# Kernel tuning notes

Measured on AMD Instinct MI355X. Metric: run time of the kernel, lower is better.

Reference implementation:

```python
import jax, jax.numpy as jnp
import numpy as np

B, S, V, E, H, L = 32, 64, 96, 256, 512, 3
DIN = 2 * H  # padded input width for stacked LSTM weight tensors


def _cell(x, h, c, Wih, Whh, bih, bhh):
    # PyTorch LSTMCell gate order: i, f, g, o
    g = x @ Wih.T + h @ Whh.T + bih + bhh
    i, f, gg, o = jnp.split(g, 4, axis=-1)
    c2 = jax.nn.sigmoid(f) * c + jax.nn.sigmoid(i) * jnp.tanh(gg)
    h2 = jax.nn.sigmoid(o) * jnp.tanh(c2)
    return h2, c2


def _pad_feat(x, d):
    p = d - x.shape[-1]
    return x if p == 0 else jnp.pad(x, ((0, 0),) * (x.ndim - 1) + ((0, p),))


def _run_lstm(xs, Wih, Whh, bih, bhh, reverse):
    # xs: [S, B, Din]
    if reverse:
        xs = xs[::-1]
    b = xs.shape[1]
    init = (jnp.zeros((b, H), xs.dtype), jnp.zeros((b, H), xs.dtype))

    def step(carry, xt):
        h, c = _cell(xt, carry[0], carry[1], Wih, Whh, bih, bhh)
        return (h, c), h

    (h, c), ys = jax.lax.scan(step, init, xs)
    if reverse:
        ys = ys[::-1]
    return ys, h, c


def setup_inputs():
    key = jax.random.key(0)
    ks = jax.random.split(key, 20)
    f = lambda k, shp, s=0.08: jax.random.normal(k, shp, jnp.float32) * s
    return {
        "src": jax.random.randint(ks[0], (B, S), 0, V - 1),  # avoids padding_idx=95
        "trg": jax.random.randint(ks[1], (B, S), 0, V - 1),
        "embedding": f(ks[2], (V, E), 0.5),
        "enc_Wih": f(ks[3], (L, 2, 4 * H, DIN)),
        "enc_Whh": f(ks[4], (L, 2, 4 * H, H)),
        "enc_bih": f(ks[5], (L, 2, 4 * H)),
        "enc_bhh": f(ks[6], (L, 2, 4 * H)),
        "dec_Wih": f(ks[7], (L, 4 * H, DIN)),
        "dec_Whh": f(ks[8], (L, 4 * H, H)),
        "dec_bih": f(ks[9], (L, 4 * H)),
        "dec_bhh": f(ks[10], (L, 4 * H)),
        "attn_W": f(ks[11], (H, 3 * H)),
        "attn_b": f(ks[12], (H,)),
        "attn_v": jax.random.uniform(ks[13], (H,), jnp.float32),
        "proj_W": f(ks[14], (2 * H, E + 2 * H)),
        "proj_b": f(ks[15], (2 * H,)),
        "fc_W": f(ks[16], (V, H)),
        "fc_b": f(ks[17], (V,)),
    }


def _forward(src, trg, embedding, enc_Wih, enc_Whh, enc_bih, enc_bhh,
             dec_Wih, dec_Whh, dec_bih, dec_bhh, attn_W, attn_b, attn_v,
             proj_W, proj_b, fc_W, fc_b):
    emb = embedding[src]                 # [B,S,E]; dropout=identity (eval)
    xs = emb.transpose(1, 0, 2)          # [S,B,E]
    h_sum, c_sum = [], []
    for l in range(L):
        xin = _pad_feat(xs, DIN)         # zero-pad so stacked weights apply; padded cols hit zeros
        yf, hf, cf = _run_lstm(xin, enc_Wih[l, 0], enc_Whh[l, 0], enc_bih[l, 0], enc_bhh[l, 0], False)
        yb, hb, cb = _run_lstm(xin, enc_Wih[l, 1], enc_Whh[l, 1], enc_bih[l, 1], enc_bhh[l, 1], True)
        xs = jnp.concatenate([yf, yb], -1)  # [S,B,2H]
        h_sum.append(hf + hb)
        c_sum.append(cf + cb)            # hidden.view(L,2,B,H).sum(dim=1)
    enc_out = xs.transpose(1, 0, 2)      # [B,S,2H]
    dec_h, dec_c = jnp.stack(h_sum), jnp.stack(c_sum)  # [L,B,H]

    tokens = trg[:, :-1].T               # teacher_forcing_ratio = 1.0 (deterministic)

    def dec_step(carry, tok):
        h, c = carry
        htop = h[-1]                     # [B,H]
        rep = jnp.concatenate([jnp.broadcast_to(htop[:, None, :], (B, S, H)), enc_out], -1)
        energy = jnp.tanh(rep @ attn_W.T + attn_b)               # [B,S,H]
        attn = jax.nn.softmax(jnp.einsum('d,bsd->bs', attn_v, energy), axis=1)
        context = jnp.einsum('bs,bsd->bd', attn, enc_out)        # [B,2H]
        x = jnp.concatenate([embedding[tok], context], -1) @ proj_W.T + proj_b  # [B,2H]
        hs, cs = [], []
        xin = x
        for l in range(L):
            hl, cl = _cell(_pad_feat(xin, DIN), h[l], c[l], dec_Wih[l], dec_Whh[l], dec_bih[l], dec_bhh[l])
            hs.append(hl)
            cs.append(cl)
            xin = hl
        out = xin @ fc_W.T + fc_b        # [B,V]
        return (jnp.stack(hs), jnp.stack(cs)), out

    _, outs = jax.lax.scan(dec_step, (dec_h, dec_c), tokens)     # [S-1,B,V]
    outputs = jnp.concatenate([jnp.zeros((1, B, V), outs.dtype), outs], 0)
    return outputs.transpose(1, 0, 2)    # [B,S,V]; t=0 row is zeros, matching torch


def reference(src, trg, embedding, enc_Wih, enc_Whh, enc_bih, enc_bhh,
              dec_Wih, dec_Whh, dec_bih, dec_bhh, attn_W, attn_b, attn_v,
              proj_W, proj_b, fc_W, fc_b):
    return _forward(src, trg, embedding, enc_Wih, enc_Whh, enc_bih, enc_bhh,
                    dec_Wih, dec_Whh, dec_bih, dec_bhh, attn_W, attn_b, attn_v,
                    proj_W, proj_b, fc_W, fc_b)
```

## Files before the change

### kernel.cpp

```cpp
#include <hip/hip_runtime.h>

#define B_ 32
#define S_ 64
#define V_ 96
#define E_ 256
#define H_ 512
#define L_ 3
#define DIN_ 1024
#define G4_ 2048
#define BH_ (B_*H_)
#define BDIN_ (B_*DIN_)
#define FSTRIDE 16

typedef unsigned short u16;

__device__ __forceinline__ float bfu(u16 u){ return __uint_as_float(((unsigned)u) << 16); }
__device__ __forceinline__ u16 f2b(float f){
  unsigned x = __float_as_uint(f);
  unsigned r = (x + 0x7FFFu + ((x >> 16) & 1u)) >> 16;
  return (u16)r;
}
__device__ __forceinline__ float sigm(float x){ return 1.f/(1.f+__expf(-x)); }
__device__ __forceinline__ float bsum(float a){
  #pragma unroll
  for(int off=1; off<64; off<<=1) a += __shfl_xor(a, off);
  return a;
}
__device__ __forceinline__ void stc(float* p, float v){
  __hip_atomic_store(p, v, __ATOMIC_RELAXED, __HIP_MEMORY_SCOPE_AGENT);
}
__device__ __forceinline__ float ldc(const float* p){
  return __hip_atomic_load((float*)p, __ATOMIC_RELAXED, __HIP_MEMORY_SCOPE_AGENT);
}
__device__ __forceinline__ void stci(int* p, int v){
  __hip_atomic_store(p, v, __ATOMIC_RELAXED, __HIP_MEMORY_SCOPE_AGENT);
}
__device__ __forceinline__ int ldci(const int* p){
  return __hip_atomic_load((int*)p, __ATOMIC_RELAXED, __HIP_MEMORY_SCOPE_AGENT);
}
template<int BF> __device__ __forceinline__ float LD(const void* p, size_t i){
  if constexpr(BF) return bfu(((const u16*)p)[i]);
  else             return ((const float*)p)[i];
}
template<int BF> __device__ __forceinline__ float4 LD4(const void* p, size_t i){
  if constexpr(BF){
    const u16* q = (const u16*)p + i;
    ushort4 w = *(const ushort4*)q;
    return make_float4(bfu(w.x), bfu(w.y), bfu(w.z), bfu(w.w));
  } else {
    return *(const float4*)((const float*)p + i);
  }
}

__device__ __forceinline__ void gbar(int* flags, int g){
  __syncthreads();
  if(threadIdx.x < 64){
    if(threadIdx.x == 0) stci(&flags[blockIdx.x*FSTRIDE], g);
    const int i0 = threadIdx.x*4;
    for(;;){
      int f0 = ldci(&flags[(i0+0)*FSTRIDE]);
      int f1 = ldci(&flags[(i0+1)*FSTRIDE]);
      int f2 = ldci(&flags[(i0+2)*FSTRIDE]);
      int f3 = ldci(&flags[(i0+3)*FSTRIDE]);
      bool ok = (f0>=g) && (f1>=g) && (f2>=g) && (f3>=g);
      if(__all(ok)) break;
      __builtin_amdgcn_s_sleep(1);
    }
  }
  __syncthreads();
}

__global__ void k_detect(const void* av, int* flag, int* flags){
  __shared__ int cnt;
  if(threadIdx.x == 0) cnt = 0;
  __syncthreads();
  u16 w = ((const u16*)av)[2*threadIdx.x];
  if(w & 0x8000) atomicAdd(&cnt, 1);
  __syncthreads();
  for(int i=threadIdx.x; i<256*FSTRIDE+16; i+=256) flags[i] = 0;
  if(threadIdx.x == 0) *flag = (cnt <= 8) ? 1 : 0;
}

template<int BF> __device__ void embed_body(const int* __restrict__ src,
                                            const void* __restrict__ emb,
                                            float* __restrict__ X0){
  int idx = blockIdx.x*256 + threadIdx.x;
  int d  = idx & (DIN_-1);
  int sb = idx >> 10;
  int b  = sb & (B_-1);
  int s  = sb >> 5;
  float v = 0.f;
  if(d < E_){
    int tok = src[b*S_ + s];
    v = LD<BF>(emb, (size_t)tok*E_ + d);
  }
  X0[idx] = v;
}
__global__ void k_embed(const int* src, const void* emb, float* X0, const int* fl){
  if(*fl) embed_body<1>(src, emb, X0); else embed_body<0>(src, emb, X0);
}

template<int BF> __device__ void gemm_body(
  const float* __restrict__ A, int lda,
  const void* __restrict__ W, int ldw, size_t woff,
  const void* __restrict__ b1, size_t o1,
  const void* __restrict__ b2, size_t o2,
  float* __restrict__ C, int ldc, int K)
{
  __shared__ float As[16][128];
  __shared__ float Bs[16][64];
  const int tid = threadIdx.x;
  const int m0 = blockIdx.y * 128;
  const int n0 = blockIdx.x * 64;
  const int tx = tid & 15, ty = tid >> 4;
  const int amm = tid & 127, akk = (tid >> 7) * 8;
  const int bnn = tid >> 2,  bkk = (tid & 3) * 4;
  float acc[8][4] = {{0.f}};
  for(int k0 = 0; k0 < K; k0 += 16){
    const float4* ap = (const float4*)(A + (size_t)(m0+amm)*lda + (k0 + akk));
    float4 a0 = ap[0];
    float4 a1 = ap[1];
    float4 wv = LD4<BF>(W, woff + (size_t)(n0+bnn)*ldw + (k0 + bkk));
    As[akk+0][amm]=a0.x; As[akk+1][amm]=a0.y; As[akk+2][amm]=a0.z; As[akk+3][amm]=a0.w;
    As[akk+4][amm]=a1.x; As[akk+5][amm]=a1.y; As[akk+6][amm]=a1.z; As[akk+7][amm]=a1.w;
    Bs[bkk+0][bnn]=wv.x; Bs[bkk+1][bnn]=wv.y;
    Bs[bkk+2][bnn]=wv.z; Bs[bkk+3][bnn]=wv.w;
    __syncthreads();
    #pragma unroll
    for(int kk=0;kk<16;kk++){
      const float4 av0 = *(const float4*)&As[kk][ty*8];
      const float4 av1 = *(const float4*)&As[kk][ty*8+4];
      const float4 bv  = *(const float4*)&Bs[kk][tx*4];
      float am[8] = {av0.x,av0.y,av0.z,av0.w,av1.x,av1.y,av1.z,av1.w};
      float bn[4] = {bv.x,bv.y,bv.z,bv.w};
      #pragma unroll
      for(int i=0;i<8;i++){
        #pragma unroll
        for(int j=0;j<4;j++) acc[i][j] = fmaf(am[i], bn[j], acc[i][j]);
      }
    }
    __syncthreads();
  }
  float bias[4];
  #pragma unroll
  for(int j=0;j<4;j++){
    float bb = 0.f;
    if(b1) bb += LD<BF>(b1, o1 + n0 + tx*4 + j);
    if(b2) bb += LD<BF>(b2, o2 + n0 + tx*4 + j);
    bias[j] = bb;
  }
  #pragma unroll
  for(int i=0;i<8;i++){
    float* cp = C + (size_t)(m0 + ty*8 + i)*ldc + (n0 + tx*4);
    #pragma unroll
    for(int j=0;j<4;j++) cp[j] = acc[i][j] + bias[j];
  }
}
__global__ __launch_bounds__(256) void k_gemm(
  const float* A, int lda, const void* W, int ldw, size_t woff,
  const void* b1, size_t o1, const void* b2, size_t o2,
  float* C, int ldc, int K, const int* fl)
{
  if(*fl) gemm_body<1>(A,lda,W,ldw,woff,b1,o1,b2,o2,C,ldc,K);
  else    gemm_body<0>(A,lda,W,ldw,woff,b1,o1,b2,o2,C,ldc,K);
}

__global__ void k_outzero(void* __restrict__ out, const int* fl){
  int i = blockIdx.x*256 + threadIdx.x;
  if(i < B_*V_){
    int b = i / V_, v = i % V_;
    size_t idx = (size_t)b*(S_*V_) + v;
    if(*fl) ((u16*)out)[idx] = 0;
    else    ((float*)out)[idx] = 0.f;
  }
}

struct EncArgs2 {
  const float* G;
  const void* Whh; size_t oWh;
  float* henc;
  float* cT;
  float* Xout;
  float* dh0;
  float* dcT;
  int l;
  const int* fl;
  int* flags; int gbase;
};

template<int BF>
__device__ void enc2_body(const EncArgs2& a){
  __shared__ float SM[16384];
  const int tid  = threadIdx.x;
  const int lane = tid & 63;
  const int wid  = tid >> 6;
  const int w4   = (blockIdx.x<<2) + (wid & 3);
  const int j    = w4 & 511;
  const int d    = w4 >> 9;
  const int half = wid >> 2;
  int g = a.gbase;

  float wh[4][8];
  #pragma unroll
  for(int gg=0; gg<4; gg++){
    size_t rowh = a.oWh + ((size_t)d*G4_ + (size_t)gg*H_ + j)*H_;
    #pragma unroll
    for(int p=0;p<2;p++){
      float4 v = LD4<BF>(a.Whh, rowh + (lane<<2) + p*256);
      wh[gg][p*4+0]=v.x; wh[gg][p*4+1]=v.y; wh[gg][p*4+2]=v.z; wh[gg][p*4+3]=v.w;
    }
  }
  const bool own = (lane < 32) && ((lane>>4) == half);
  const size_t ci = ((size_t)d*H_ + j)*32 + (lane & 31);
  float cv = 0.f;

  for(int p=0;p<64;p++){
    const int t = d ? (63-p) : p;
    if(p == 0){
      for(int i=tid<<2; i<BH_; i+=2048) *(float4*)&SM[i] = make_float4(0.f,0.f,0.f,0.f);
    } else {
      const float* hsrc = a.henc + (size_t)((p&63)*2 + d)*BH_;
      for(int i=tid<<2; i<BH_; i+=2048) *(float4*)&SM[i] = *(const float4*)&hsrc[i];
    }
    __syncthreads();

    const int bE = lane & 31;
    const float* Gp = a.G + (size_t)(t*B_+bE)*4096 + (size_t)d*G4_ + j;
    float pg0=Gp[0], pg1=Gp[512], pg2=Gp[1024], pg3=Gp[1536];

    float gv0=0.f, gv1=0.f, gv2=0.f, gv3=0.f;
    for(int b=half*16; b<half*16+16; b++){
      float gs[4] = {0.f,0.f,0.f,0.f};
      const float* hp = &SM[(b<<9) + (lane<<2)];
      #pragma unroll
      for(int pp=0;pp<2;pp++){
        float4 hv = *(const float4*)(hp + pp*256);
        float ha[4] = {hv.x,hv.y,hv.z,hv.w};
        #pragma unroll
        for(int gg=0;gg<4;gg++){
          #pragma unroll
          for(int i=0;i<4;i++) gs[gg] = fmaf(ha[i], wh[gg][pp*4+i], gs[gg]);
        }
      }
      #pragma unroll
      for(int gg=0;gg<4;gg++) gs[gg] = bsum(gs[gg]);
      if(lane == b){ gv0=gs[0]; gv1=gs[1]; gv2=gs[2]; gv3=gs[3]; }
    }
    if(own){
      float gi = gv0+pg0, gf = gv1+pg1, gG = gv2+pg2, go = gv3+pg3;
      float c2 = sigm(gf)*cv + sigm(gi)*tanhf(gG);
      float h2 = sigm(go)*tanhf(c2);
      cv = c2;
      stc(&a.henc[(size_t)(((p+1)&63)*2 + d)*BH_ + (size_t)lane*H_ + j], h2);
      a.Xout[(size_t)(t*B_+lane)*DIN_ + (d<<9) + j] = h2;
    }
    gbar(a.flags, ++g);
  }
  if(own) stc(&a.cT[ci], cv);
  gbar(a.flags, ++g);
  for(int i = blockIdx.x*512 + tid; i < BH_; i += 131072){
    float hf2 = a.henc[(size_t)(0*2+0)*BH_ + i];
    float hb2 = a.henc[(size_t)(0*2+1)*BH_ + i];
    a.dh0[(size_t)a.l*BH_ + i] = hf2 + hb2;
    a.dcT[(size_t)a.l*BH_ + i] = ldc(&a.cT[i]) + ldc(&a.cT[BH_ + i]);
  }
}
__global__ __launch_bounds__(512,1) void k_enc2(EncArgs2 a){
  if(*a.fl) enc2_body<1>(a); else enc2_body<0>(a);
}

struct DecArgs2 {
  const int* trg;
  const void* emb; const void* aW; const void* av; const void* pW; const void* pb;
  const void* dWih; const void* dWhh; const void* dbih; const void* dbhh;
  const void* fW; const void* fb;
  const float* Epre; const float* X3;
  const float* dh0;
  float* dhb;
  float* zb;
  u16*   ctxb;
  float* xpb;
  const float* dcT;
  void* out;
  const int* fl;
  int* flags; int gbase;
};

template<int BF, int CP>
__device__ __forceinline__ void dec_loadW(const DecArgs2& a, const int l,
    const int jp, const int lane, const int half,
    float wx[2][16], float wh[2][8], float pg[2]){
  #pragma unroll
  for(int gg=0; gg<2; gg++){
    const int gr = half*2 + gg;
    size_t rowx = ((size_t)l*G4_ + (size_t)gr*H_ + jp)*DIN_;
    #pragma unroll
    for(int p=0;p<CP;p++){
      float4 v = LD4<BF>(a.dWih, rowx + (lane<<2) + p*256);
      wx[gg][p*4+0]=v.x; wx[gg][p*4+1]=v.y; wx[gg][p*4+2]=v.z; wx[gg][p*4+3]=v.w;
    }
    size_t rowh = ((size_t)l*G4_ + (size_t)gr*H_ + jp)*H_;
    #pragma unroll
    for(int p=0;p<2;p++){
      float4 v = LD4<BF>(a.dWhh, rowh + (lane<<2) + p*256);
      wh[gg][p*4+0]=v.x; wh[gg][p*4+1]=v.y; wh[gg][p*4+2]=v.z; wh[gg][p*4+3]=v.w;
    }
    size_t bb = (size_t)l*G4_ + (size_t)gr*H_ + jp;
    pg[gg] = LD<BF>(a.dbih, bb) + LD<BF>(a.dbhh, bb);
  }
}

template<int BF, int CP>
__device__ __forceinline__ void dec_cellG(const DecArgs2& a, float* SM,
    const int t, const int l, const int jp, const int bh, const int bh_blk,
    const int lane, const int tid, const int half, const int pairid,
    float wx[2][16], float wh[2][8], float pg[2], float& cv){
  constexpr int Kx  = CP*256;
  constexpr int HB  = (CP==4) ? 2 : 1;
  constexpr int NBs = 16/HB;
  const float* xsrc = (l==0) ? (a.xpb + (size_t)t*BDIN_ + (size_t)bh_blk*16*DIN_)
                             : (a.dhb + (size_t)((t+1)*3 + (l-1))*BH_ + (size_t)bh_blk*16*H_);
  const float* hsrc = (t==0) ? (a.dh0 + (size_t)l*BH_ + (size_t)bh_blk*16*H_)
                             : (a.dhb + (size_t)(t*3 + l)*BH_ + (size_t)bh_blk*16*H_);
  float gvA=0.f, gvB=0.f;
  #pragma unroll
  for(int hf=0; hf<HB; hf++){
    const float* xg = xsrc + (size_t)hf*NBs*Kx;
    const float* hg = hsrc + (size_t)hf*NBs*H_;
    for(int i=tid<<2; i<NBs*Kx; i+=2048) *(float4*)&SM[i] = *(const float4*)&xg[i];
    for(int i=tid<<2; i<NBs*H_; i+=2048) *(float4*)&SM[NBs*Kx + i] = *(const float4*)&hg[i];
    __syncthreads();
    for(int ib2=0; ib2<NBs; ib2++){
      const int ib = hf*NBs + ib2;
      float gs0=0.f, gs1=0.f;
      const float* xr = &SM[ib2*Kx + (lane<<2)];
      #pragma unroll
      for(int p=0;p<CP;p++){
        float4 xv = *(const float4*)(xr + p*256);
        gs0 = fmaf(xv.x, wx[0][p*4+0], gs0); gs0 = fmaf(xv.y, wx[0][p*4+1], gs0);
        gs0 = fmaf(xv.z, wx[0][p*4+2], gs0); gs0 = fmaf(xv.w, wx[0][p*4+3], gs0);
        gs1 = fmaf(xv.x, wx[1][p*4+0], gs1); gs1 = fmaf(xv.y, wx[1][p*4+1], gs1);
        gs1 = fmaf(xv.z, wx[1][p*4+2], gs1); gs1 = fmaf(xv.w, wx[1][p*4+3], gs1);
      }
      const float* hr = &SM[NBs*Kx + ib2*H_ + (lane<<2)];
      #pragma unroll
      for(int p=0;p<2;p++){
        float4 hv = *(const float4*)(hr + p*256);
        gs0 = fmaf(hv.x, wh[0][p*4+0], gs0); gs0 = fmaf(hv.y, wh[0][p*4+1], gs0);
        gs0 = fmaf(hv.z, wh[0][p*4+2], gs0); gs0 = fmaf(hv.w, wh[0][p*4+3], gs0);
        gs1 = fmaf(hv.x, wh[1][p*4+0], gs1); gs1 = fmaf(hv.y, wh[1][p*4+1], gs1);
        gs1 = fmaf(hv.z, wh[1][p*4+2], gs1); gs1 = fmaf(hv.w, wh[1][p*4+3], gs1);
      }
      gs0 = bsum(gs0); gs1 = bsum(gs1);
      if(lane == ib){ gvA=gs0; gvB=gs1; }
    }
    __syncthreads();
  }
  float* comb = SM + 15360 + pairid*128;
  if(lane < 16){
    comb[half*32 + lane*2 + 0] = gvA + pg[0];
    comb[half*32 + lane*2 + 1] = gvB + pg[1];
  }
  __syncthreads();
  if(half == 0 && lane < 16){
    const int b = bh*16 + lane;
    float gi = comb[lane*2 + 0];
    float gf = comb[lane*2 + 1];
    float gG = comb[32 + lane*2 + 0];
    float go = comb[32 + lane*2 + 1];
    float c2 = sigm(gf)*cv + sigm(gi)*tanhf(gG);
    float h2 = sigm(go)*tanhf(c2);
    cv = c2;
    stc(&a.dhb[(size_t)((t+1)*3 + l)*BH_ + (size_t)b*H_ + jp], h2);
  }
}

template<int BF>
__device__ void dec2_body(const DecArgs2& a){
  __shared__ float SM[16384];
  const int tid  = threadIdx.x;
  const int lane = tid & 63;
  const int wid  = tid >> 6;
  const int w4   = (blockIdx.x<<2) + (wid & 3);
  const int jp   = w4 & 511;
  const int bh   = w4 >> 9;
  const int half = wid >> 2;
  const int pairid = wid & 3;
  const int bh_blk = blockIdx.x >> 7;
  int g = a.gbase;

  float cvs[3];
  #pragma unroll
  for(int l=0;l<3;l++)
    cvs[l] = a.dcT[((size_t)l*H_ + jp)*32 + (size_t)bh*16 + (lane&15)];

  float wx[2][16], wh[2][8], pg[2];

  for(int t=0; t<64; ++t){
    {
      const float* hs = (t==0) ? (a.dh0 + (size_t)2*BH_ + (size_t)bh_blk*16*H_)
                               : (a.dhb + (size_t)(t*3 + 2)*BH_ + (size_t)bh_blk*16*H_);
      for(int i=tid<<2; i<16*H_; i+=2048) *(float4*)&SM[i] = *(const float4*)&hs[i];
      __syncthreads();
      if(t < 63){
        float wz[8];
        size_t rz = (size_t)jp*1536;
        #pragma unroll
        for(int p=0;p<2;p++){
          float4 v = LD4<BF>(a.aW, rz + (lane<<2) + p*256);
          wz[p*4+0]=v.x; wz[p*4+1]=v.y; wz[p*4+2]=v.z; wz[p*4+3]=v.w;
        }
        for(int ib=half*8; ib<half*8+8; ib++){
          const float* hp = &SM[(ib<<9) + (lane<<2)];
          float acc = 0.f;
          #pragma unroll
          for(int p=0;p<2;p++){
            float4 hv = *(const float4*)(hp + p*256);
            acc = fmaf(hv.x, wz[p*4+0], acc); acc = fmaf(hv.y, wz[p*4+1], acc);
            acc = fmaf(hv.z, wz[p*4+2], acc); acc = fmaf(hv.w, wz[p*4+3], acc);
          }
          acc = bsum(acc);
          if(lane==0) stc(&a.zb[(size_t)t*BH_ + (size_t)(bh*16+ib)*H_ + jp], acc);
        }
      }
      if(t > 0){
        #pragma unroll
        for(int r=0;r<3;r++){
          const int q  = jp + (r<<9);
          const int v_ = q % 96;
          const int ib = q / 96;
          if((ib>>3) != half) continue;
          float wf[8];
          size_t rf = (size_t)v_*H_;
          #pragma unroll
          for(int p=0;p<2;p++){
            float4 v = LD4<BF>(a.fW, rf + (lane<<2) + p*256);
            wf[p*4+0]=v.x; wf[p*4+1]=v.y; wf[p*4+2]=v.z; wf[p*4+3]=v.w;
          }
          const float* hp = &SM[(ib<<9) + (lane<<2)];
          float acc = 0.f;
          #pragma unroll
          for(int p=0;p<2;p++){
            float4 hv = *(const float4*)(hp + p*256);
            acc = fmaf(hv.x, wf[p*4+0], acc); acc = fmaf(hv.y, wf[p*4+1], acc);
            acc = fmaf(hv.z, wf[p*4+2], acc); acc = fmaf(hv.w, wf[p*4+3], acc);
          }
          acc = bsum(acc);
          if(lane==0){
            float rr = acc + LD<BF>(a.fb, v_);
            size_t oi = (size_t)(bh*16+ib)*(S_*V_) + (size_t)t*V_ + v_;
            if constexpr(BF) ((u16*)a.out)[oi] = f2b(rr);
            else             ((float*)a.out)[oi] = rr;
          }
        }
      }
    }
    if(t == 63) break;
    gbar(a.flags, ++g);

    if(blockIdx.x < 32){
      const int b = blockIdx.x;
      float* Zs = SM; float* Ss = SM + 512;
      for(int i=tid; i<512; i+=512) Zs[i] = a.zb[(size_t)t*BH_ + (size_t)b*H_ + i];
      __syncthreads();
      float wa[8];
      #pragma unroll
      for(int p=0;p<2;p++){
        float4 v = LD4<BF>(a.av, (lane<<2) + p*256);
        wa[p*4+0]=v.x; wa[p*4+1]=v.y; wa[p*4+2]=v.z; wa[p*4+3]=v.w;
      }
      for(int s=wid; s<64; s+=8){
        const float* ep = a.Epre + ((size_t)(s*B_ + b))*H_;
        float acc = 0.f;
        #pragma unroll
        for(int p=0;p<2;p++){
          const float4 e4 = *(const float4*)(ep + (lane<<2) + p*256);
          const float4 z4 = *(const float4*)(Zs + (lane<<2) + p*256);
          acc = fmaf(wa[p*4+0], tanhf(e4.x+z4.x), acc);
          acc = fmaf(wa[p*4+1], tanhf(e4.y+z4.y), acc);
          acc = fmaf(wa[p*4+2], tanhf(e4.z+z4.z), acc);
          acc = fmaf(wa[p*4+3], tanhf(e4.w+z4.w), acc);
        }
        acc = bsum(acc);
        if(lane==0) Ss[s] = acc;
      }
      __syncthreads();
      if(tid < 64){
        float vv = Ss[tid];
        float m = vv;
        #pragma unroll
        for(int off=1; off<64; off<<=1) m = fmaxf(m, __shfl_xor(m, off));
        float e = __expf(vv - m);
        float su = e;
        #pragma unroll
        for(int off=1; off<64; off<<=1) su += __shfl_xor(su, off);
        Ss[tid] = e / su;
      }
      __syncthreads();
      for(int d4 = tid<<2; d4 < DIN_; d4 += 2048){
        float a0=0.f,a1=0.f,a2=0.f,a3=0.f;
        const float* xb = a.X3 + (size_t)b*DIN_ + d4;
        for(int s=0;s<64;s++){
          const float pp = Ss[s];
          const float4 xv = *(const float4*)(xb + (size_t)s*BDIN_);
          a0 = fmaf(pp, xv.x, a0); a1 = fmaf(pp, xv.y, a1);
          a2 = fmaf(pp, xv.z, a2); a3 = fmaf(pp, xv.w, a3);
        }
        u16* cp = a.ctxb + (size_t)t*BDIN_ + (size_t)b*DIN_ + d4;
        unsigned lo = (unsigned)f2b(a0) | ((unsigned)f2b(a1)<<16);
        unsigned hi = (unsigned)f2b(a2) | ((unsigned)f2b(a3)<<16);
        stci((int*)cp, (int)lo);
        stci(((int*)cp)+1, (int)hi);
      }
    }
    gbar(a.flags, ++g);

    {
      const u16* cs = a.ctxb + (size_t)t*BDIN_ + (size_t)bh_blk*16*DIN_;
      for(int i=tid*4; i<16*DIN_; i+=2048){
        ushort4 v = *(const ushort4*)(cs + i);
        *(float4*)&SM[i] = make_float4(bfu(v.x), bfu(v.y), bfu(v.z), bfu(v.w));
      }
      __syncthreads();
      float wpe[2][4], wpc[2][16];
      #pragma unroll
      for(int jj=0;jj<2;jj++){
        size_t row = (size_t)(jp + (jj<<9))*1280;
        float4 v = LD4<BF>(a.pW, row + (lane<<2));
        wpe[jj][0]=v.x; wpe[jj][1]=v.y; wpe[jj][2]=v.z; wpe[jj][3]=v.w;
        #pragma unroll
        for(int p=0;p<4;p++){
          float4 c4 = LD4<BF>(a.pW, row + 256 + (lane<<2) + p*256);
          wpc[jj][p*4+0]=c4.x; wpc[jj][p*4+1]=c4.y; wpc[jj][p*4+2]=c4.z; wpc[jj][p*4+3]=c4.w;
        }
      }
      const float pb0 = LD<BF>(a.pb, jp);
      const float pb1 = LD<BF>(a.pb, jp+512);
      for(int ib=half*8; ib<half*8+8; ib++){
        const int b = bh*16 + ib;
        const int tok = a.trg[b*S_ + t];
        float4 ev = LD4<BF>(a.emb, (size_t)tok*E_ + (lane<<2));
        float ea[4] = {ev.x, ev.y, ev.z, ev.w};
        float s0=0.f, s1=0.f;
        #pragma unroll
        for(int i=0;i<4;i++){ s0 = fmaf(ea[i], wpe[0][i], s0); s1 = fmaf(ea[i], wpe[1][i], s1); }
        const float* cp = &SM[(ib<<10) + (lane<<2)];
        #pragma unroll
        for(int p=0;p<4;p++){
          float4 c4 = *(const float4*)(cp + p*256);
          float ca[4] = {c4.x,c4.y,c4.z,c4.w};
          #pragma unroll
          for(int i=0;i<4;i++){ s0 = fmaf(ca[i], wpc[0][p*4+i], s0); s1 = fmaf(ca[i], wpc[1][p*4+i], s1); }
        }
        s0 = bsum(s0); s1 = bsum(s1);
        if(lane==0){
          stc(&a.xpb[(size_t)t*BDIN_ + (size_t)b*DIN_ + jp],       s0 + pb0);
          stc(&a.xpb[(size_t)t*BDIN_ + (size_t)b*DIN_ + jp + 512], s1 + pb1);
        }
      }
      __syncthreads();
    }
    dec_loadW<BF,4>(a, 0, jp, lane, half, wx, wh, pg);
    gbar(a.flags, ++g);
    dec_cellG<BF,4>(a, SM, t, 0, jp, bh, bh_blk, lane, tid, half, pairid, wx, wh, pg, cvs[0]);
    dec_loadW<BF,2>(a, 1, jp, lane, half, wx, wh, pg);
    gbar(a.flags, ++g);
    dec_cellG<BF,2>(a, SM, t, 1, jp, bh, bh_blk, lane, tid, half, pairid, wx, wh, pg, cvs[1]);
    dec_loadW<BF,2>(a, 2, jp, lane, half, wx, wh, pg);
    gbar(a.flags, ++g);
    dec_cellG<BF,2>(a, SM, t, 2, jp, bh, bh_blk, lane, tid, half, pairid, wx, wh, pg, cvs[2]);
    gbar(a.flags, ++g);
  }
}
__global__ __launch_bounds__(512,1) void k_dec2(DecArgs2 a){
  if(*a.fl) dec2_body<1>(a); else dec2_body<0>(a);
}

struct EncArgsO {
  const float* G;
  const float* Xin;
  const void* Wih; size_t oWi;
  const void* Whh; size_t oWh;
  const void* bih; size_t obi;
  const void* bhh; size_t obh;
  float* hst; float* cT; float* Xout; float* dh; float* dcT;
  int l; const int* fl; int* flags; int gbase;
};

template<int BF, int CP>
__device__ void encO_body(const EncArgsO& a){
  __shared__ float SM[16384];
  const int tid  = threadIdx.x;
  const int w    = (blockIdx.x<<2) + (tid>>6);
  const int lane = tid & 63;
  const int d    = w >> 9;
  const int j    = w & 511;
  int g = a.gbase;

  float wh[4][8];
  #pragma unroll
  for(int gg=0; gg<4; gg++){
    size_t rowh = a.oWh + ((size_t)d*G4_ + (size_t)gg*H_ + j)*H_;
    #pragma unroll
    for(int p=0;p<2;p++){
      float4 v = LD4<BF>(a.Whh, rowh + (lane<<2) + p*256);
      wh[gg][p*4+0]=v.x; wh[gg][p*4+1]=v.y; wh[gg][p*4+2]=v.z; wh[gg][p*4+3]=v.w;
    }
  }
  float wxf[4][CP?CP*4:1];
  float pbias[4];
  if constexpr(CP>0){
    #pragma unroll
    for(int gg=0; gg<4; gg++){
      size_t rowx = a.oWi + ((size_t)d*G4_ + (size_t)gg*H_ + j)*DIN_;
      #pragma unroll
      for(int p=0;p<CP;p++){
        float4 v = LD4<BF>(a.Wih, rowx + (lane<<2) + p*256);
        wxf[gg][p*4+0]=v.x; wxf[gg][p*4+1]=v.y; wxf[gg][p*4+2]=v.z; wxf[gg][p*4+3]=v.w;
      }
    }
    size_t bb = (size_t)d*G4_ + j;
    #pragma unroll
    for(int gg=0;gg<4;gg++)
      pbias[gg] = LD<BF>(a.bih, a.obi + bb + (size_t)gg*H_)
                + LD<BF>(a.bhh, a.obh + bb + (size_t)gg*H_);
  }
  const int bE = lane & 31;
  const size_t ci = ((size_t)d*H_ + j)*32 + bE;
  float cv = 0.f;
  int cur = 0;
  for(int p=0;p<64;p++){
    const int t = d ? (63-p) : p;
    if(p == 0){
      for(int i=tid<<2; i<BH_; i+=1024) *(float4*)&SM[i] = make_float4(0.f,0.f,0.f,0.f);
    } else {
      const float* hsrc = a.hst + (size_t)((cur<<1)+d)*BH_;
      #pragma unroll 4
      for(int i=tid; i<BH_; i+=256) SM[i] = ldc(hsrc + i);
    }
    __syncthreads();
    float pg[4];
    if constexpr(CP==0){
      const float* Gp = a.G + (size_t)(t*B_+bE)*4096 + (size_t)d*G4_ + j;
      pg[0]=Gp[0]; pg[1]=Gp[512]; pg[2]=Gp[1024]; pg[3]=Gp[1536];
    } else {
      pg[0]=pbias[0]; pg[1]=pbias[1]; pg[2]=pbias[2]; pg[3]=pbias[3];
    }
    const float* xrow = nullptr;
    if constexpr(CP>0) xrow = a.Xin + (size_t)t*B_*DIN_;
    float gv0=0.f, gv1=0.f, gv2=0.f, gv3=0.f;
    for(int b=0;b<32;b++){
      float gs[4] = {0.f,0.f,0.f,0.f};
      const float* hp = &SM[(b<<9) + (lane<<2)];
      #pragma unroll
      for(int pp=0;pp<2;pp++){
        float4 hv = *(const float4*)(hp + pp*256);
        float ha[4] = {hv.x,hv.y,hv.z,hv.w};
        #pragma unroll
        for(int gg=0;gg<4;gg++){
          #pragma unroll
          for(int i=0;i<4;i++) gs[gg] = fmaf(ha[i], wh[gg][pp*4+i], gs[gg]);
        }
      }
      if constexpr(CP>0){
        const float* xr = xrow + (size_t)b*DIN_ + (lane<<2);
        #pragma unroll
        for(int pp=0;pp<CP;pp++){
          float4 xv = *(const float4*)(xr + pp*256);
          float xa[4] = {xv.x,xv.y,xv.z,xv.w};
          #pragma unroll
          for(int gg=0;gg<4;gg++){
            #pragma unroll
            for(int i=0;i<4;i++) gs[gg] = fmaf(xa[i], wxf[gg][pp*4+i], gs[gg]);
          }
        }
      }
      #pragma unroll
      for(int gg=0;gg<4;gg++) gs[gg] = bsum(gs[gg]);
      if(lane == b){ gv0=gs[0]; gv1=gs[1]; gv2=gs[2]; gv3=gs[3]; }
    }
    if(lane < 32){
      float gi = gv0+pg[0], gf = gv1+pg[1], gG = gv2+pg[2], go = gv3+pg[3];
      float c2 = sigm(gf)*cv + sigm(gi)*tanhf(gG);
      float h2 = sigm(go)*tanhf(c2);
      cv = c2;
      stc(&a.hst[(size_t)(((cur^1)<<1)+d)*BH_ + (size_t)bE*H_ + j], h2);
      a.Xout[(size_t)(t*B_+bE)*DIN_ + (d<<9) + j] = h2;
    }
    gbar(a.flags, ++g);
    cur ^= 1;
  }
  if(lane < 32) stc(&a.cT[ci], cv);
  gbar(a.flags, ++g);
  for(int i = blockIdx.x*256 + tid; i < BH_; i += 65536){
    a.dh[(size_t)a.l*BH_ + i]  = ldc(&a.hst[(size_t)(cur<<1)*BH_ + i])
                               + ldc(&a.hst[(size_t)((cur<<1)+1)*BH_ + i]);
    a.dcT[(size_t)a.l*BH_ + i] = ldc(&a.cT[i]) + ldc(&a.cT[BH_ + i]);
  }
}
__global__ __launch_bounds__(256,2) void k_enc_persF0(EncArgsO a){
  if(*a.fl) encO_body<1,1>(a); else encO_body<0,1>(a);
}
__global__ __launch_bounds__(256,2) void k_enc_persF12(EncArgsO a){
  if(*a.fl) encO_body<1,4>(a); else encO_body<0,4>(a);
}

struct DecArgsO {
  const int* trg;
  const void* emb; const void* aW; const void* av; const void* pW; const void* pb;
  const void* dWih; const void* dWhh; const void* dbih; const void* dbhh;
  const void* fW; const void* fb;
  const float* Epre; const float* X3;
  float* dh; float* dcT; float* z; float* ctx; float* xp;
  void* out; const int* fl; int* flags; int gbase;
};

template<int BF, int CP>
__device__ __forceinline__ void decO_cell(const DecArgsO& a, float* SM,
    const int l, const int cur, const int jp, const int bh, const int bh_blk,
    const int lane, const int tid, int& g, float& cv){
  constexpr int Kx = CP*256;
  constexpr int HB = (CP==4) ? 2 : 1;
  constexpr int NB = 16/HB;
  const float* xsrc = (l==0) ? (a.xp + (size_t)bh_blk*16*DIN_)
                             : (a.dh + ((size_t)(cur^1)*3 + (l-1))*BH_ + (size_t)bh_blk*16*H_);
  const float* hsrc = a.dh + ((size_t)cur*3 + l)*BH_ + (size_t)bh_blk*16*H_;
  float wx[4][CP*4];
  float wh[4][8];
  #pragma unroll
  for(int gg=0; gg<4; gg++){
    size_t rowx = ((size_t)l*G4_ + (size_t)gg*H_ + jp)*DIN_;
    #pragma unroll
    for(int p=0;p<CP;p++){
      float4 v = LD4<BF>(a.dWih, rowx + (lane<<2) + p*256);
      wx[gg][p*4+0]=v.x; wx[gg][p*4+1]=v.y; wx[gg][p*4+2]=v.z; wx[gg][p*4+3]=v.w;
    }
    size_t rowh = ((size_t)l*G4_ + (size_t)gg*H_ + jp)*H_;
    #pragma unroll
    for(int p=0;p<2;p++){
      float4 v = LD4<BF>(a.dWhh, rowh + (lane<<2) + p*256);
      wh[gg][p*4+0]=v.x; wh[gg][p*4+1]=v.y; wh[gg][p*4+2]=v.z; wh[gg][p*4+3]=v.w;
    }
  }
  float pg[4];
  {
    size_t bb = (size_t)l*G4_ + jp;
    #pragma unroll
    for(int gg=0;gg<4;gg++)
      pg[gg] = LD<BF>(a.dbih, bb + (size_t)gg*H_) + LD<BF>(a.dbhh, bb + (size_t)gg*H_);
  }
  float gv0=0.f,gv1=0.f,gv2=0.f,gv3=0.f;
  #pragma unroll
  for(int hf=0; hf<HB; hf++){
    const float* xg = xsrc + (size_t)hf*NB*Kx;
    const float* hg = hsrc + (size_t)hf*NB*H_;
    #pragma unroll 4
    for(int i=tid; i<NB*Kx; i+=256) SM[i] = ldc(xg + i);
    #pragma unroll 4
    for(int i=tid; i<NB*H_; i+=256) SM[NB*Kx + i] = ldc(hg + i);
    __syncthreads();
    for(int ib2=0; ib2<NB; ib2++){
      const int ib = hf*NB + ib2;
      float gs[4] = {0.f,0.f,0.f,0.f};
      const float* xr = &SM[ib2*Kx + (lane<<2)];
      #pragma unroll
      for(int p=0;p<CP;p++){
        float4 xv = *(const float4*)(xr + p*256);
        float xa[4] = {xv.x,xv.y,xv.z,xv.w};
        #pragma unroll
        for(int gg=0;gg<4;gg++){
          #pragma unroll
          for(int i=0;i<4;i++) gs[gg] = fmaf(xa[i], wx[gg][p*4+i], gs[gg]);
        }
      }
      const float* hr = &SM[NB*Kx + ib2*H_ + (lane<<2)];
      #pragma unroll
      for(int p=0;p<2;p++){
        float4 hv = *(const float4*)(hr + p*256);
        float ha[4] = {hv.x,hv.y,hv.z,hv.w};
        #pragma unroll
        for(int gg=0;gg<4;gg++){
          #pragma unroll
          for(int i=0;i<4;i++) gs[gg] = fmaf(ha[i], wh[gg][p*4+i], gs[gg]);
        }
      }
      #pragma unroll
      for(int gg=0;gg<4;gg++) gs[gg] = bsum(gs[gg]);
      if(lane == ib){ gv0=gs[0]; gv1=gs[1]; gv2=gs[2]; gv3=gs[3]; }
    }
    __syncthreads();
  }
  if(lane < 16){
    const int b = bh*16 + lane;
    float gi = gv0+pg[0], gf = gv1+pg[1], gG = gv2+pg[2], go = gv3+pg[3];
    float c2 = sigm(gf)*cv + sigm(gi)*tanhf(gG);
    float h2 = sigm(go)*tanhf(c2);
    cv = c2;
    stc(&a.dh[((size_t)(cur^1)*3 + l)*BH_ + (size_t)b*H_ + jp], h2);
  }
  gbar(a.flags, ++g);
}

template<int BF>
__device__ void decO_body(const DecArgsO& a){
  __shared__ float SM[16384];
  const int tid  = threadIdx.x;
  const int w    = (blockIdx.x<<2) + (tid>>6);
  const int lane = tid & 63;
  const int jp   = w & 511;
  const int bh   = w >> 9;
  const int bh_blk = blockIdx.x >> 7;
  int g = a.gbase;
  float cvs[3];
  #pragma unroll
  for(int l=0;l<3;l++)
    cvs[l] = a.dcT[((size_t)l*H_ + jp)*32 + (size_t)bh*16 + (lane&15)];
  int cur = 0;
  for(int t=0; t<64; ++t){
    {
      const float* hs = a.dh + ((size_t)cur*3 + 2)*BH_ + (size_t)bh_blk*16*H_;
      #pragma unroll 4
      for(int i=tid; i<16*H_; i+=256) SM[i] = ldc(hs + i);
      __syncthreads();
      if(t < 63){
        float wz[8];
        size_t rz = (size_t)jp*1536;
        #pragma unroll
        for(int p=0;p<2;p++){
          float4 v = LD4<BF>(a.aW, rz + (lane<<2) + p*256);
          wz[p*4+0]=v.x; wz[p*4+1]=v.y; wz[p*4+2]=v.z; wz[p*4+3]=v.w;
        }
        for(int ib=0; ib<16; ib++){
          const float* hp = &SM[(ib<<9) + (lane<<2)];
          float acc = 0.f;
          #pragma unroll
          for(int p=0;p<2;p++){
            float4 hv = *(const float4*)(hp + p*256);
            acc = fmaf(hv.x, wz[p*4+0], acc); acc = fmaf(hv.y, wz[p*4+1], acc);
            acc = fmaf(hv.z, wz[p*4+2], acc); acc = fmaf(hv.w, wz[p*4+3], acc);
          }
          acc = bsum(acc);
          if(lane==0) stc(&a.z[(size_t)(bh*16+ib)*H_ + jp], acc);
        }
      }
      if(t > 0){
        #pragma unroll
        for(int r=0;r<3;r++){
          const int q  = jp + (r<<9);
          const int v_ = q % 96;
          const int ib = q / 96;
          float wf[8];
          size_t rf = (size_t)v_*H_;
          #pragma unroll
          for(int p=0;p<2;p++){
            float4 v = LD4<BF>(a.fW, rf + (lane<<2) + p*256);
            wf[p*4+0]=v.x; wf[p*4+1]=v.y; wf[p*4+2]=v.z; wf[p*4+3]=v.w;
          }
          const float* hp = &SM[(ib<<9) + (lane<<2)];
          float acc = 0.f;
          #pragma unroll
          for(int p=0;p<2;p++){
            float4 hv = *(const float4*)(hp + p*256);
            acc = fmaf(hv.x, wf[p*4+0], acc); acc = fmaf(hv.y, wf[p*4+1], acc);
            acc = fmaf(hv.z, wf[p*4+2], acc); acc = fmaf(hv.w, wf[p*4+3], acc);
          }
          acc = bsum(acc);
          if(lane==0){
            float rr = acc + LD<BF>(a.fb, v_);
            size_t oi = (size_t)(bh*16+ib)*(S_*V_) + (size_t)t*V_ + v_;
            if constexpr(BF) ((u16*)a.out)[oi] = f2b(rr);
            else             ((float*)a.out)[oi] = rr;
          }
        }
      }
    }
    if(t == 63) break;
    gbar(a.flags, ++g);
    if(blockIdx.x < 32){
      const int b = blockIdx.x;
      float* Zs = SM; float* Ss = SM + 512;
      for(int i=tid; i<512; i+=256) Zs[i] = ldc(a.z + (size_t)b*H_ + i);
      __syncthreads();
      float wa[8];
      #pragma unroll
      for(int p=0;p<2;p++){
        float4 v = LD4<BF>(a.av, (lane<<2) + p*256);
        wa[p*4+0]=v.x; wa[p*4+1]=v.y; wa[p*4+2]=v.z; wa[p*4+3]=v.w;
      }
      const int ww = tid>>6;
      for(int s=ww; s<64; s+=4){
        const float* ep = a.Epre + ((size_t)(s*B_ + b))*H_;
        float acc = 0.f;
        #pragma unroll
        for(int p=0;p<2;p++){
          const float4 e4 = *(const float4*)(ep + (lane<<2) + p*256);
          const float4 z4 = *(const float4*)(Zs + (lane<<2) + p*256);
          acc = fmaf(wa[p*4+0], tanhf(e4.x+z4.x), acc);
          acc = fmaf(wa[p*4+1], tanhf(e4.y+z4.y), acc);
          acc = fmaf(wa[p*4+2], tanhf(e4.z+z4.z), acc);
          acc = fmaf(wa[p*4+3], tanhf(e4.w+z4.w), acc);
        }
        acc = bsum(acc);
        if(lane==0) Ss[s] = acc;
      }
      __syncthreads();
      if(tid < 64){
        float vv = Ss[tid];
        float m = vv;
        #pragma unroll
        for(int off=1; off<64; off<<=1) m = fmaxf(m, __shfl_xor(m, off));
        float e = __expf(vv - m);
        float su = e;
        #pragma unroll
        for(int off=1; off<64; off<<=1) su += __shfl_xor(su, off);
        Ss[tid] = e / su;
      }
      __syncthreads();
      for(int d4 = tid<<2; d4 < DIN_; d4 += 1024){
        float a0=0.f,a1=0.f,a2=0.f,a3=0.f;
        const float* xb = a.X3 + (size_t)b*DIN_ + d4;
        for(int s=0;s<64;s++){
          const float pp = Ss[s];
          const float4 xv = *(const float4*)(xb + (size_t)s*BDIN_);
          a0 = fmaf(pp, xv.x, a0); a1 = fmaf(pp, xv.y, a1);
          a2 = fmaf(pp, xv.z, a2); a3 = fmaf(pp, xv.w, a3);
        }
        float* cp = &a.ctx[(size_t)b*DIN_ + d4];
        stc(cp+0, a0); stc(cp+1, a1); stc(cp+2, a2); stc(cp+3, a3);
      }
    }
    gbar(a.flags, ++g);
    {
      const float* cs = a.ctx + (size_t)bh_blk*16*DIN_;
      #pragma unroll 4
      for(int i=tid; i<16*DIN_; i+=256) SM[i] = ldc(cs + i);
      __syncthreads();
      float wpe[2][4], wpc[2][16];
      #pragma unroll
      for(int jj=0;jj<2;jj++){
        size_t row = (size_t)(jp + (jj<<9))*1280;
        float4 v = LD4<BF>(a.pW, row + (lane<<2));
        wpe[jj][0]=v.x; wpe[jj][1]=v.y; wpe[jj][2]=v.z; wpe[jj][3]=v.w;
        #pragma unroll
        for(int p=0;p<4;p++){
          float4 c4 = LD4<BF>(a.pW, row + 256 + (lane<<2) + p*256);
          wpc[jj][p*4+0]=c4.x; wpc[jj][p*4+1]=c4.y; wpc[jj][p*4+2]=c4.z; wpc[jj][p*4+3]=c4.w;
        }
      }
      const float pb0 = LD<BF>(a.pb, jp);
      const float pb1 = LD<BF>(a.pb, jp+512);
      for(int ib=0; ib<16; ib++){
        const int b = bh*16 + ib;
        const int tok = a.trg[b*S_ + t];
        float4 ev = LD4<BF>(a.emb, (size_t)tok*E_ + (lane<<2));
        float ea[4] = {ev.x, ev.y, ev.z, ev.w};
        float s0=0.f, s1=0.f;
        #pragma unroll
        for(int i=0;i<4;i++){ s0 = fmaf(ea[i], wpe[0][i], s0); s1 = fmaf(ea[i], wpe[1][i], s1); }
        const float* cp = &SM[(ib<<10) + (lane<<2)];
        #pragma unroll
        for(int p=0;p<4;p++){
          float4 c4 = *(const float4*)(cp + p*256);
          float ca[4] = {c4.x,c4.y,c4.z,c4.w};
          #pragma unroll
          for(int i=0;i<4;i++){ s0 = fmaf(ca[i], wpc[0][p*4+i], s0); s1 = fmaf(ca[i], wpc[1][p*4+i], s1); }
        }
        s0 = bsum(s0); s1 = bsum(s1);
        if(lane==0){
          stc(&a.xp[(size_t)b*DIN_ + jp],       s0 + pb0);
          stc(&a.xp[(size_t)b*DIN_ + jp + 512], s1 + pb1);
        }
      }
    }
    gbar(a.flags, ++g);
    decO_cell<BF,4>(a, SM, 0, cur, jp, bh, bh_blk, lane, tid, g, cvs[0]);
    decO_cell<BF,2>(a, SM, 1, cur, jp, bh, bh_blk, lane, tid, g, cvs[1]);
    decO_cell<BF,2>(a, SM, 2, cur, jp, bh, bh_blk, lane, tid, g, cvs[2]);
    cur ^= 1;
  }
}
__global__ __launch_bounds__(256,2) void k_dec_persO(DecArgsO a){
  if(*a.fl) decO_body<1>(a); else decO_body<0>(a);
}

extern "C" void kernel_launch(void* const* d_in, const int* in_sizes, int n_in,
                              void* d_out, int out_size, void* d_ws, size_t ws_size,
                              hipStream_t stream){
  const int* src  = (const int*)d_in[0];
  const int* trg  = (const int*)d_in[1];
  const void* emb = d_in[2];
  const void* eWih= d_in[3];
  const void* eWhh= d_in[4];
  const void* ebih= d_in[5];
  const void* ebhh= d_in[6];
  const void* dWih= d_in[7];
  const void* dWhh= d_in[8];
  const void* dbih= d_in[9];
  const void* dbhh= d_in[10];
  const void* aW  = d_in[11];
  const void* ab  = d_in[12];
  const void* av  = d_in[13];
  const void* pW  = d_in[14];
  const void* pb  = d_in[15];
  const void* fW  = d_in[16];
  const void* fb  = d_in[17];

  char* base = (char*)d_ws;
  size_t off = 0;
  auto take = [&](size_t bytes)->char*{
    char* p = base + off; off = (off + bytes + 255) & ~(size_t)255; return p;
  };

  const size_t szX  = (size_t)2048*1024*4;
  const size_t szG  = (size_t)2048*4096*4;
  const size_t szE  = (size_t)2048*512*4;
  int planA = ws_size >= (size_t)53*1024*1024;

  if(planA){
    float* X    = (float*)take(szX);
    float* Xh   = (float*)take(szX);
    float* G    = (float*)take(szG);
    float* dhb  = G;
    float* zb   = dhb + (size_t)64*3*BH_;
    float* xpb  = zb  + (size_t)63*BH_;
    u16*   ctxb = (u16*)(xpb + (size_t)63*BDIN_);
    float* Epre = (float*)take(szE);
    float* cTe  = (float*)take((size_t)2*BH_*4);
    float* dh0  = (float*)take((size_t)3*BH_*4);
    float* dcT  = (float*)take((size_t)3*BH_*4);
    int* fl     = (int*)take(256);
    int* flags  = (int*)take((256*FSTRIDE + 16)*4);

    k_detect<<<1, 256, 0, stream>>>(av, fl, flags);
    k_embed<<<8192, 256, 0, stream>>>(src, emb, X, fl);

    for(int l=0;l<L_;l++){
      int K = (l==0) ? E_ : DIN_;
      k_gemm<<<dim3(64,16), 256, 0, stream>>>(X, DIN_,
          eWih, DIN_, (size_t)l*2*G4_*DIN_,
          ebih, (size_t)l*2*G4_, ebhh, (size_t)l*2*G4_,
          G, 4096, K, fl);
      EncArgs2 ea;
      ea.G = G; ea.Whh = eWhh; ea.oWh = (size_t)l*2*G4_*H_;
      ea.henc = Xh; ea.cT = cTe; ea.Xout = X;
      ea.dh0 = dh0; ea.dcT = dcT; ea.l = l;
      ea.fl = fl; ea.flags = flags; ea.gbase = l*65;
      k_enc2<<<256, 512, 0, stream>>>(ea);
    }
    k_gemm<<<dim3(8,16), 256, 0, stream>>>(X, DIN_,
        aW, 3*H_, (size_t)H_, ab, 0, nullptr, 0, Epre, H_, DIN_, fl);
    k_outzero<<<12, 256, 0, stream>>>(d_out, fl);

    DecArgs2 da;
    da.trg = trg; da.emb = emb; da.aW = aW; da.av = av; da.pW = pW; da.pb = pb;
    da.dWih = dWih; da.dWhh = dWhh; da.dbih = dbih; da.dbhh = dbhh;
    da.fW = fW; da.fb = fb;
    da.Epre = Epre; da.X3 = X;
    da.dh0 = dh0; da.dhb = dhb; da.zb = zb; da.ctxb = ctxb; da.xpb = xpb;
    da.dcT = dcT; da.out = d_out; da.fl = fl; da.flags = flags; da.gbase = 3*65;
    k_dec2<<<256, 512, 0, stream>>>(da);
  } else {
    float* XA   = (float*)take(szX);
    float* XB   = (float*)take(szX);
    float* Epre = (float*)take(szE);
    float* hst  = (float*)take((size_t)4*BH_*4);
    float* cTe  = (float*)take((size_t)2*BH_*4);
    float* dh   = (float*)take((size_t)6*BH_*4);
    float* dcT  = (float*)take((size_t)3*BH_*4);
    float* zbuf = (float*)take((size_t)BH_*4);
    float* ctx  = (float*)take((size_t)2*BH_*4);
    float* xp   = (float*)take((size_t)2*BH_*4);
    int* fl     = (int*)take(256);
    int* flags  = (int*)take((256*FSTRIDE + 16)*4);

    k_detect<<<1, 256, 0, stream>>>(av, fl, flags);
    k_embed<<<8192, 256, 0, stream>>>(src, emb, XA, fl);

    float* Xin = XA; float* Xout = XB;
    for(int l=0;l<L_;l++){
      EncArgsO ea;
      ea.G = nullptr; ea.Xin = Xin;
      ea.Wih = eWih; ea.oWi = (size_t)l*2*G4_*DIN_;
      ea.Whh = eWhh; ea.oWh = (size_t)l*2*G4_*H_;
      ea.bih = ebih; ea.obi = (size_t)l*2*G4_;
      ea.bhh = ebhh; ea.obh = (size_t)l*2*G4_;
      ea.hst = hst; ea.cT = cTe; ea.Xout = Xout;
      ea.dh = dh; ea.dcT = dcT; ea.l = l;
      ea.fl = fl; ea.flags = flags; ea.gbase = l*65;
      if(l == 0) k_enc_persF0<<<256, 256, 0, stream>>>(ea);
      else       k_enc_persF12<<<256, 256, 0, stream>>>(ea);
      float* tmp = Xin; Xin = Xout; Xout = tmp;
    }
    k_gemm<<<dim3(8,16), 256, 0, stream>>>(Xin, DIN_,
        aW, 3*H_, (size_t)H_, ab, 0, nullptr, 0, Epre, H_, DIN_, fl);
    k_outzero<<<12, 256, 0, stream>>>(d_out, fl);

    DecArgsO da;
    da.trg = trg; da.emb = emb; da.aW = aW; da.av = av; da.pW = pW; da.pb = pb;
    da.dWih = dWih; da.dWhh = dWhh; da.dbih = dbih; da.dbhh = dbhh;
    da.fW = fW; da.fb = fb;
    da.Epre = Epre; da.X3 = Xin;
    da.dh = dh; da.dcT = dcT; da.z = zbuf; da.ctx = ctx; da.xp = xp;
    da.out = d_out; da.fl = fl; da.flags = flags; da.gbase = 3*65;
    k_dec_persO<<<256, 256, 0, stream>>>(da);
  }
}
```

Baseline: 9.584 ms.

## Split attention context across all blocks and break FMA dependency chains

The attention/context phase previously ran on only 32 blocks (one per batch row). It now runs on every block (b = blockIdx>>3, 8 slices of the 1024-wide context), so each block recomputes the scores and softmax but accumulates only 128 context columns. This is meant to shorten the serial context phase between global barriers, at the cost of redundant score work. Several dot products (gate, attention-z, fc, projection) also switch to two independent accumulators to shorten FMA dependency chains, which changes the summation order slightly.

```diff
diff --git a/kernel.cpp b/kernel.cpp
--- a/kernel.cpp
+++ b/kernel.cpp
@@ -332,26 +332,40 @@
     __syncthreads();
     for(int ib2=0; ib2<NBs; ib2++){
       const int ib = hf*NBs + ib2;
-      float gs0=0.f, gs1=0.f;
+      float g0a=0.f,g0b=0.f,g1a=0.f,g1b=0.f;
       const float* xr = &SM[ib2*Kx + (lane<<2)];
       #pragma unroll
       for(int p=0;p<CP;p++){
         float4 xv = *(const float4*)(xr + p*256);
-        gs0 = fmaf(xv.x, wx[0][p*4+0], gs0); gs0 = fmaf(xv.y, wx[0][p*4+1], gs0);
-        gs0 = fmaf(xv.z, wx[0][p*4+2], gs0); gs0 = fmaf(xv.w, wx[0][p*4+3], gs0);
-        gs1 = fmaf(xv.x, wx[1][p*4+0], gs1); gs1 = fmaf(xv.y, wx[1][p*4+1], gs1);
-        gs1 = fmaf(xv.z, wx[1][p*4+2], gs1); gs1 = fmaf(xv.w, wx[1][p*4+3], gs1);
+        if(p & 1){
+          g0b = fmaf(xv.x, wx[0][p*4+0], g0b); g0b = fmaf(xv.y, wx[0][p*4+1], g0b);
+          g0b = fmaf(xv.z, wx[0][p*4+2], g0b); g0b = fmaf(xv.w, wx[0][p*4+3], g0b);
+          g1b = fmaf(xv.x, wx[1][p*4+0], g1b); g1b = fmaf(xv.y, wx[1][p*4+1], g1b);
+          g1b = fmaf(xv.z, wx[1][p*4+2], g1b); g1b = fmaf(xv.w, wx[1][p*4+3], g1b);
+        } else {
+          g0a = fmaf(xv.x, wx[0][p*4+0], g0a); g0a = fmaf(xv.y, wx[0][p*4+1], g0a);
+          g0a = fmaf(xv.z, wx[0][p*4+2], g0a); g0a = fmaf(xv.w, wx[0][p*4+3], g0a);
+          g1a = fmaf(xv.x, wx[1][p*4+0], g1a); g1a = fmaf(xv.y, wx[1][p*4+1], g1a);
+          g1a = fmaf(xv.z, wx[1][p*4+2], g1a); g1a = fmaf(xv.w, wx[1][p*4+3], g1a);
+        }
       }
       const float* hr = &SM[NBs*Kx + ib2*H_ + (lane<<2)];
-      #pragma unroll
-      for(int p=0;p<2;p++){
-        float4 hv = *(const float4*)(hr + p*256);
-        gs0 = fmaf(hv.x, wh[0][p*4+0], gs0); gs0 = fmaf(hv.y, wh[0][p*4+1], gs0);
-        gs0 = fmaf(hv.z, wh[0][p*4+2], gs0); gs0 = fmaf(hv.w, wh[0][p*4+3], gs0);
-        gs1 = fmaf(hv.x, wh[1][p*4+0], gs1); gs1 = fmaf(hv.y, wh[1][p*4+1], gs1);
-        gs1 = fmaf(hv.z, wh[1][p*4+2], gs1); gs1 = fmaf(hv.w, wh[1][p*4+3], gs1);
-      }
-      gs0 = bsum(gs0); gs1 = bsum(gs1);
+      {
+        float4 hv = *(const float4*)(hr);
+        g0a = fmaf(hv.x, wh[0][0], g0a); g0a = fmaf(hv.y, wh[0][1], g0a);
+        g0a = fmaf(hv.z, wh[0][2], g0a); g0a = fmaf(hv.w, wh[0][3], g0a);
+        g1a = fmaf(hv.x, wh[1][0], g1a); g1a = fmaf(hv.y, wh[1][1], g1a);
+        g1a = fmaf(hv.z, wh[1][2], g1a); g1a = fmaf(hv.w, wh[1][3], g1a);
+      }
+      {
+        float4 hv = *(const float4*)(hr + 256);
+        g0b = fmaf(hv.x, wh[0][4], g0b); g0b = fmaf(hv.y, wh[0][5], g0b);
+        g0b = fmaf(hv.z, wh[0][6], g0b); g0b = fmaf(hv.w, wh[0][7], g0b);
+        g1b = fmaf(hv.x, wh[1][4], g1b); g1b = fmaf(hv.y, wh[1][5], g1b);
+        g1b = fmaf(hv.z, wh[1][6], g1b); g1b = fmaf(hv.w, wh[1][7], g1b);
+      }
+      float gs0 = bsum(g0a + g0b);
+      float gs1 = bsum(g1a + g1b);
       if(lane == ib){ gvA=gs0; gvB=gs1; }
     }
     __syncthreads();
@@ -412,14 +426,18 @@
         }
         for(int ib=half*8; ib<half*8+8; ib++){
           const float* hp = &SM[(ib<<9) + (lane<<2)];
-          float acc = 0.f;
-          #pragma unroll
-          for(int p=0;p<2;p++){
-            float4 hv = *(const float4*)(hp + p*256);
-            acc = fmaf(hv.x, wz[p*4+0], acc); acc = fmaf(hv.y, wz[p*4+1], acc);
-            acc = fmaf(hv.z, wz[p*4+2], acc); acc = fmaf(hv.w, wz[p*4+3], acc);
+          float aa = 0.f, ab = 0.f;
+          {
+            float4 hv = *(const float4*)(hp);
+            aa = fmaf(hv.x, wz[0], aa); aa = fmaf(hv.y, wz[1], aa);
+            aa = fmaf(hv.z, wz[2], aa); aa = fmaf(hv.w, wz[3], aa);
           }
-          acc = bsum(acc);
+          {
+            float4 hv = *(const float4*)(hp + 256);
+            ab = fmaf(hv.x, wz[4], ab); ab = fmaf(hv.y, wz[5], ab);
+            ab = fmaf(hv.z, wz[6], ab); ab = fmaf(hv.w, wz[7], ab);
+          }
+          float acc = bsum(aa + ab);
           if(lane==0) stc(&a.zb[(size_t)t*BH_ + (size_t)(bh*16+ib)*H_ + jp], acc);
         }
       }
@@ -438,14 +456,18 @@
             wf[p*4+0]=v.x; wf[p*4+1]=v.y; wf[p*4+2]=v.z; wf[p*4+3]=v.w;
           }
           const float* hp = &SM[(ib<<9) + (lane<<2)];
-          float acc = 0.f;
-          #pragma unroll
-          for(int p=0;p<2;p++){
-            float4 hv = *(const float4*)(hp + p*256);
-            acc = fmaf(hv.x, wf[p*4+0], acc); acc = fmaf(hv.y, wf[p*4+1], acc);
-            acc = fmaf(hv.z, wf[p*4+2], acc); acc = fmaf(hv.w, wf[p*4+3], acc);
+          float aa = 0.f, ab = 0.f;
+          {
+            float4 hv = *(const float4*)(hp);
+            aa = fmaf(hv.x, wf[0], aa); aa = fmaf(hv.y, wf[1], aa);
+            aa = fmaf(hv.z, wf[2], aa); aa = fmaf(hv.w, wf[3], aa);
           }
-          acc = bsum(acc);
+          {
+            float4 hv = *(const float4*)(hp + 256);
+            ab = fmaf(hv.x, wf[4], ab); ab = fmaf(hv.y, wf[5], ab);
+            ab = fmaf(hv.z, wf[6], ab); ab = fmaf(hv.w, wf[7], ab);
+          }
+          float acc = bsum(aa + ab);
           if(lane==0){
             float rr = acc + LD<BF>(a.fb, v_);
             size_t oi = (size_t)(bh*16+ib)*(S_*V_) + (size_t)t*V_ + v_;
@@ -458,10 +480,11 @@
     if(t == 63) break;
     gbar(a.flags, ++g);
 
-    if(blockIdx.x < 32){
-      const int b = blockIdx.x;
+    {
+      const int b  = blockIdx.x >> 3;
+      const int ss = blockIdx.x & 7;
       float* Zs = SM; float* Ss = SM + 512;
-      for(int i=tid; i<512; i+=512) Zs[i] = a.zb[(size_t)t*BH_ + (size_t)b*H_ + i];
+      Zs[tid] = a.zb[(size_t)t*BH_ + (size_t)b*H_ + tid];
       __syncthreads();
       float wa[8];
       #pragma unroll
@@ -497,15 +520,22 @@
         Ss[tid] = e / su;
       }
       __syncthreads();
-      for(int d4 = tid<<2; d4 < DIN_; d4 += 2048){
+      if(tid < 32){
+        const int d4 = ss*128 + (tid<<2);
         float a0=0.f,a1=0.f,a2=0.f,a3=0.f;
+        float b0=0.f,b1=0.f,b2=0.f,b3=0.f;
         const float* xb = a.X3 + (size_t)b*DIN_ + d4;
-        for(int s=0;s<64;s++){
+        for(int s=0;s<64;s+=2){
           const float pp = Ss[s];
+          const float qq = Ss[s+1];
           const float4 xv = *(const float4*)(xb + (size_t)s*BDIN_);
+          const float4 yv = *(const float4*)(xb + (size_t)(s+1)*BDIN_);
           a0 = fmaf(pp, xv.x, a0); a1 = fmaf(pp, xv.y, a1);
           a2 = fmaf(pp, xv.z, a2); a3 = fmaf(pp, xv.w, a3);
-        }
+          b0 = fmaf(qq, yv.x, b0); b1 = fmaf(qq, yv.y, b1);
+          b2 = fmaf(qq, yv.z, b2); b3 = fmaf(qq, yv.w, b3);
+        }
+        a0 += b0; a1 += b1; a2 += b2; a3 += b3;
         u16* cp = a.ctxb + (size_t)t*BDIN_ + (size_t)b*DIN_ + d4;
         unsigned lo = (unsigned)f2b(a0) | ((unsigned)f2b(a1)<<16);
         unsigned hi = (unsigned)f2b(a2) | ((unsigned)f2b(a3)<<16);
@@ -540,19 +570,29 @@
         const int b = bh*16 + ib;
         const int tok = a.trg[b*S_ + t];
         float4 ev = LD4<BF>(a.emb, (size_t)tok*E_ + (lane<<2));
-        float ea[4] = {ev.x, ev.y, ev.z, ev.w};
-        float s0=0.f, s1=0.f;
-        #pragma unroll
-        for(int i=0;i<4;i++){ s0 = fmaf(ea[i], wpe[0][i], s0); s1 = fmaf(ea[i], wpe[1][i], s1); }
+        float s0a=0.f, s0b=0.f, s1a=0.f, s1b=0.f;
+        s0a = fmaf(ev.x, wpe[0][0], s0a); s0a = fmaf(ev.y, wpe[0][1], s0a);
+        s0a = fmaf(ev.z, wpe[0][2], s0a); s0a = fmaf(ev.w, wpe[0][3], s0a);
+        s1a = fmaf(ev.x, wpe[1][0], s1a); s1a = fmaf(ev.y, wpe[1][1], s1a);
+        s1a = fmaf(ev.z, wpe[1][2], s1a); s1a = fmaf(ev.w, wpe[1][3], s1a);
         const float* cp = &SM[(ib<<10) + (lane<<2)];
         #pragma unroll
         for(int p=0;p<4;p++){
           float4 c4 = *(const float4*)(cp + p*256);
-          float ca[4] = {c4.x,c4.y,c4.z,c4.w};
-          #pragma unroll
-          for(int i=0;i<4;i++){ s0 = fmaf(ca[i], wpc[0][p*4+i], s0); s1 = fmaf(ca[i], wpc[1][p*4+i], s1); }
-        }
-        s0 = bsum(s0); s1 = bsum(s1);
+          if(p & 1){
+            s0b = fmaf(c4.x, wpc[0][p*4+0], s0b); s0b = fmaf(c4.y, wpc[0][p*4+1], s0b);
+            s0b = fmaf(c4.z, wpc[0][p*4+2], s0b); s0b = fmaf(c4.w, wpc[0][p*4+3], s0b);
+            s1b = fmaf(c4.x, wpc[1][p*4+0], s1b); s1b = fmaf(c4.y, wpc[1][p*4+1], s1b);
+            s1b = fmaf(c4.z, wpc[1][p*4+2], s1b); s1b = fmaf(c4.w, wpc[1][p*4+3], s1b);
+          } else {
+            s0a = fmaf(c4.x, wpc[0][p*4+0], s0a); s0a = fmaf(c4.y, wpc[0][p*4+1], s0a);
+            s0a = fmaf(c4.z, wpc[0][p*4+2], s0a); s0a = fmaf(c4.w, wpc[0][p*4+3], s0a);
+            s1a = fmaf(c4.x, wpc[1][p*4+0], s1a); s1a = fmaf(c4.y, wpc[1][p*4+1], s1a);
+            s1a = fmaf(c4.z, wpc[1][p*4+2], s1a); s1a = fmaf(c4.w, wpc[1][p*4+3], s1a);
+          }
+        }
+        float s0 = bsum(s0a + s0b);
+        float s1 = bsum(s1a + s1b);
         if(lane==0){
           stc(&a.xpb[(size_t)t*BDIN_ + (size_t)b*DIN_ + jp],       s0 + pb0);
           stc(&a.xpb[(size_t)t*BDIN_ + (size_t)b*DIN_ + jp + 512], s1 + pb1);
```

Measured after the change: 9.570 ms. No clear change (-0.1%).
